# Performance work log

Measured on AMD Instinct MI355X. Metric: run time of the kernel, lower is better.

The kernel has to match this reference:

```python
import jax, jax.numpy as jnp
import numpy as np

HEAD_DIM = 16

def setup_inputs() -> dict:
    key = jax.random.key(0)
    ks = jax.random.split(key, 9)
    dim = 256
    B, H, W = 8, 32, 32
    x  = jax.random.normal(ks[0], (B, H, W, dim), jnp.float32)
    # Conv2d weights in OIHW layout (torch convention), small init
    w3 = jax.random.normal(ks[1], (dim, dim, 1, 1), jnp.float32) * 0.05
    b3 = jax.random.normal(ks[2], (dim,), jnp.float32) * 0.01
    w5 = jax.random.normal(ks[3], (dim, dim, 3, 3), jnp.float32) * 0.02
    b5 = jax.random.normal(ks[4], (dim,), jnp.float32) * 0.01
    w7 = jax.random.normal(ks[5], (dim, dim, 5, 5), jnp.float32) * 0.01
    b7 = jax.random.normal(ks[6], (dim,), jnp.float32) * 0.01
    # nn.Linear weight: (out_features=dim, in_features=attention_dim=dim), no bias
    wp = jax.random.normal(ks[7], (dim, dim), jnp.float32) * 0.05
    return {"x": x, "w3": w3, "b3": b3, "w5": w5, "b5": b5, "w7": w7, "b7": b7, "wp": wp}

def _conv2d_same(x_nchw, w_oihw, b):
    y = jax.lax.conv_general_dilated(
        x_nchw, w_oihw, window_strides=(1, 1), padding='SAME',
        dimension_numbers=('NCHW', 'OIHW', 'NCHW'))
    return y + b[None, :, None, None]

def reference(x, w3, b3, w5, b5, w7, b7, wp):
    B, H, W, C = x.shape
    N = H * W
    nh = C // HEAD_DIM            # num_heads
    scale = HEAD_DIM ** (-0.5)
    xc = jnp.transpose(x, (0, 3, 1, 2))  # NCHW
    # q: 1x1 conv, v: 3x3 conv, k: 5x5 conv (names match the torch code)
    q = _conv2d_same(xc, w3, b3).reshape(B, nh, N, HEAD_DIM)
    v = _conv2d_same(xc, w5, b5).reshape(B, nh, N, HEAD_DIM)
    k = _conv2d_same(xc, w7, b7).reshape(B, nh, N, HEAD_DIM)
    attn = jax.nn.softmax(jnp.einsum('bhnd,bhmd->bhnm', q, k) * scale, axis=-1)
    out = jnp.einsum('bhnm,bhmd->bhnd', attn, v)        # [B, nh, N, hd]
    out = jnp.transpose(out, (0, 2, 1, 3)).reshape(B, H, W, nh * HEAD_DIM)
    return out @ wp.T                                   # Linear, no bias
```

## Files before the change

### kernel.cpp

```cpp
#include <hip/hip_runtime.h>
#include <hip/hip_bf16.h>

#define DIM 256
#define HW  1024

typedef __attribute__((ext_vector_type(8))) short short8;
typedef __attribute__((ext_vector_type(4))) float floatx4;
typedef __attribute__((ext_vector_type(16))) float floatx16;
typedef __attribute__((address_space(1))) const unsigned int g_u32;
typedef __attribute__((address_space(3))) unsigned int l_u32;

#define QSCALE 0.36067376022224085f

__device__ inline unsigned short f2bf(float f) {
  union { float f; unsigned u; } v;
  v.f = f;
  unsigned u = v.u;
  u += 0x7fffu + ((u >> 16) & 1u);
  return (unsigned short)(u >> 16);
}

__device__ inline unsigned short f2bf_trunc(float f) {
  union { float f; unsigned u; } v;
  v.f = f;
  return (unsigned short)(v.u >> 16);
}

__device__ inline float ldin(const void* p, long i, int isf32) {
  if (isf32) return ((const float*)p)[i];
  union { unsigned u; float f; } v;
  v.u = ((unsigned)((const unsigned short*)p)[i]) << 16;
  return v.f;
}

__device__ inline int detect_inline(const unsigned short* __restrict__ xr,
                                    int* cnt) {
  if (threadIdx.x == 0) *cnt = 0;
  __syncthreads();
  int local = 0;
  for (int i = threadIdx.x; i < 8192; i += 256) {
    unsigned short u = xr[i];
    if ((u & 0x7F80u) == 0x7F80u) local++;
  }
  if (local) atomicAdd(cnt, local);
  __syncthreads();
  return (*cnt > 0) ? 1 : 0;
}

__device__ inline void frag_repack4(const void* __restrict__ w,
                                    unsigned short* __restrict__ wF, int KK,
                                    int slice, float* __restrict__ Wl,
                                    int isf32) {
  const int t = threadIdx.x;
  const int co16 = slice & 15;
  const int c8   = slice >> 4;
  const int RE = 32 * KK;
  const int RS = RE + 1;
  for (int g = 0; g < 4; ++g) {
    __syncthreads();
    for (int rloc = 0; rloc < 4; ++rloc) {
      const long base =
          ((long)((co16 * 16 + (g << 2) + rloc) * 256 + c8 * 32)) * KK;
      for (int i = t; i < RE; i += 256)
        Wl[rloc * RS + i] = ldin(w, base + i, isf32);
    }
    __syncthreads();
    for (int tap = 0; tap < KK; ++tap) {
      unsigned short* dst = wF + ((((tap << 3) + c8) << 4) + co16) * 512;
      if (t < 128) {
        const int colg = t >> 5;
        const int cis  = t & 31;
        const int col  = (g << 2) + colg;
        const int lane = ((cis >> 3) << 4) | col;
        const int j    = cis & 7;
        dst[lane * 8 + j] = f2bf(Wl[colg * RS + cis * KK + tap]);
      }
    }
  }
}

__global__ __launch_bounds__(256) void prep_kernel(
    const void* __restrict__ x,  const void* __restrict__ w3,
    const void* __restrict__ b3, const void* __restrict__ w5,
    const void* __restrict__ b5, const void* __restrict__ w7,
    const void* __restrict__ b7, const void* __restrict__ wp,
    unsigned short* __restrict__ xbf,
    unsigned short* __restrict__ wF3, unsigned short* __restrict__ wF5,
    unsigned short* __restrict__ wF7, unsigned short* __restrict__ wpF,
    float* __restrict__ bc, int* __restrict__ flag) {
  __shared__ float Wl[4 * 801];
  __shared__ int cnt;
  const int isf32 = detect_inline((const unsigned short*)x, &cnt);
  const int bid = blockIdx.x;
  const int t = threadIdx.x;
  if (bid < 512) {
#pragma unroll
    for (int r = 0; r < 4; ++r) {
      const int i = (bid * 1024 + r * 256 + t) * 4;
      if (isf32) {
        const float4 v = *(const float4*)((const float*)x + i);
        ushort4 o;
        o.x = f2bf(v.x); o.y = f2bf(v.y); o.z = f2bf(v.z); o.w = f2bf(v.w);
        *(ushort4*)(xbf + i) = o;
      } else {
        *(ushort4*)(xbf + i) =
            *(const ushort4*)((const unsigned short*)x + i);
      }
    }
  } else if (bid < 640) {
    frag_repack4(w7, wF7, 25, bid - 512, Wl, isf32);
  } else if (bid < 768) {
    frag_repack4(w5, wF5, 9, bid - 640, Wl, isf32);
  } else if (bid < 896) {
    frag_repack4(w3, wF3, 1, bid - 768, Wl, isf32);
  } else if (bid < 1024) {
    frag_repack4(wp, wpF, 1, bid - 896, Wl, isf32);
  } else {
#pragma unroll
    for (int r = 0; r < 3; ++r) {
      const int i = r * 256 + t;
      const void* src = (i < 256) ? b3 : (i < 512) ? b5 : b7;
      bc[i] = ldin(src, i & 255, isf32);
    }
    if (t == 0) *flag = isf32;
  }
}

__global__ __launch_bounds__(256, 2) void convqkv_kernel(
    const unsigned short* __restrict__ xbf,
    const unsigned short* __restrict__ wFq,
    const unsigned short* __restrict__ wFv,
    const unsigned short* __restrict__ wFk,
    const float* __restrict__ bc,
    unsigned short* __restrict__ qOut,
    unsigned short* __restrict__ vOut,
    unsigned short* __restrict__ kOut) {
  constexpr int WC = 36;
  constexpr int CELLS = 12 * WC;
  constexpr int LOADS = CELLS * 4;
  __shared__ unsigned short Xs[CELLS * 40];
  __shared__ unsigned short Bs[36 * 512];
  const int t    = threadIdx.x;
  const int bid  = blockIdx.x;
  const int cog0 = bid & 15;
  const int co0  = cog0 << 4;
  const int m0   = (bid >> 4) << 8;
  const int b    = m0 >> 10;
  const int n0   = m0 & 1023;
  const int r0   = n0 >> 5;
  const int wv   = t >> 6;
  const int lane = t & 63;
  const int l15  = lane & 15;
  const int quad = lane >> 4;

  floatx4 aq[4] = {}, av[4] = {}, ak[4] = {};

  for (int c8 = 0; c8 < 8; ++c8) {
    uint4 xreg[7];
#pragma unroll
    for (int rr = 0; rr < 7; ++rr) {
      const int id = rr * 256 + t;
      const int cell = id >> 2, part = id & 3;
      const int hr = cell / WC, wc = cell - hr * WC;
      const int xr = r0 + hr - 2, xc = wc - 2;
      const bool ok = (id < LOADS) && ((unsigned)xr < 32u) &&
                      ((unsigned)xc < 32u);
      const int cr = xr < 0 ? 0 : (xr > 31 ? 31 : xr);
      const int cc = xc < 0 ? 0 : (xc > 31 ? 31 : xc);
      uint4 v = *(const uint4*)&xbf[(((b * 32 + cr) * 32 + cc) << 8) +
                                    (c8 << 5) + (part << 3)];
      if (!ok) v = make_uint4(0, 0, 0, 0);
      xreg[rr] = v;
    }
    __syncthreads();
#pragma unroll
    for (int rr = 0; rr < 9; ++rr) {
      const int tap = (rr << 2) + wv;
      if (tap < 35) {
        const unsigned short* src;
        if (tap < 25) {
          src = &wFk[((((tap << 3) + c8) << 4) + cog0) * 512];
        } else if (tap < 34) {
          src = &wFv[(((((tap - 25) << 3) + c8) << 4) + cog0) * 512];
        } else {
          src = &wFq[((c8 << 4) + cog0) * 512];
        }
        __builtin_amdgcn_global_load_lds((g_u32*)(src + (lane << 3)),
                                         (l_u32*)&Bs[tap << 9], 16, 0, 0);
      }
    }
#pragma unroll
    for (int rr = 0; rr < 7; ++rr) {
      const int id = rr * 256 + t;
      if (id < LOADS)
        *(uint4*)&Xs[(id >> 2) * 40 + ((id & 3) << 3)] = xreg[rr];
    }
    __syncthreads();

#pragma unroll
    for (int tap = 0; tap < 25; ++tap) {
      const int kh = tap / 5, kw = tap % 5;
      const bool vv = (kh >= 1 && kh <= 3 && kw >= 1 && kw <= 3);
      short8 a[4];
#pragma unroll
      for (int rr2 = 0; rr2 < 2; ++rr2) {
#pragma unroll
        for (int ch = 0; ch < 2; ++ch) {
          const unsigned short* xs =
              &Xs[(((wv << 1) + rr2 + kh) * WC + (ch << 4) + l15 + kw) * 40 +
                  (quad << 3)];
          a[(rr2 << 1) + ch] = *(const short8*)xs;
        }
      }
      const short8 kb = *(const short8*)&Bs[(tap << 9) + (lane << 3)];
#pragma unroll
      for (int f = 0; f < 4; ++f)
        ak[f] = __builtin_amdgcn_mfma_f32_16x16x32_bf16(a[f], kb, ak[f],
                                                        0, 0, 0);
      if (vv) {
        const int vt = (kh - 1) * 3 + (kw - 1);
        const short8 vb = *(const short8*)&Bs[((25 + vt) << 9) + (lane << 3)];
#pragma unroll
        for (int f = 0; f < 4; ++f)
          av[f] = __builtin_amdgcn_mfma_f32_16x16x32_bf16(a[f], vb, av[f],
                                                          0, 0, 0);
      }
      if (tap == 12) {
        const short8 qb = *(const short8*)&Bs[(34 << 9) + (lane << 3)];
#pragma unroll
        for (int f = 0; f < 4; ++f)
          aq[f] = __builtin_amdgcn_mfma_f32_16x16x32_bf16(a[f], qb, aq[f],
                                                          0, 0, 0);
      }
    }
  }
#pragma unroll
  for (int rr2 = 0; rr2 < 2; ++rr2) {
#pragma unroll
    for (int ch = 0; ch < 2; ++ch) {
      const int f = (rr2 << 1) + ch;
      const int co = co0 + l15;
      const int slab = (b << 4) + (co >> 4);
      const int clo = co & 15;
      const int nb = n0 + (wv << 6) + (rr2 << 5) + (ch << 4) + (quad << 2);
      {
        const float bj = bc[co];
        floatx4 a = aq[f];
        ushort4 pk4;
        pk4.x = f2bf((a[0] + bj) * QSCALE);
        pk4.y = f2bf((a[1] + bj) * QSCALE);
        pk4.z = f2bf((a[2] + bj) * QSCALE);
        pk4.w = f2bf((a[3] + bj) * QSCALE);
        *(ushort4*)&qOut[(slab << 14) + (clo << 10) + nb] = pk4;
      }
      {
        const float bj = bc[512 + co];
        floatx4 a = ak[f];
        ushort4 pk4;
        pk4.x = f2bf(a[0] + bj); pk4.y = f2bf(a[1] + bj);
        pk4.z = f2bf(a[2] + bj); pk4.w = f2bf(a[3] + bj);
        *(ushort4*)&kOut[(slab << 14) + (clo << 10) + nb] = pk4;
      }
      {
        const float bj = bc[256 + co];
        floatx4 a = av[f];
        const int base = (slab << 14) + (clo << 6);
#pragma unroll
        for (int i = 0; i < 4; ++i) {
          const int n = nb + i;
          vOut[base + ((n & 15) << 10) + (n >> 4)] = f2bf(a[i] + bj);
        }
      }
    }
  }
}

__global__ __launch_bounds__(256, 4) void attn_mfma_kernel(
    const unsigned short* __restrict__ qg,
    const unsigned short* __restrict__ kg,
    const unsigned short* __restrict__ vg,
    unsigned short* __restrict__ out2) {
  __shared__ __align__(16) unsigned short Pb[4][32][40];
  const int t    = threadIdx.x;
  const int w    = t >> 6;
  const int lane = t & 63;
  const int slab = blockIdx.x >> 3;
  const int rb   = blockIdx.x & 7;
  const int b = slab >> 4;
  const int h = slab & 15;
  const int l31  = lane & 31;
  const int hl   = lane >> 5;
  const int l15  = lane & 15;
  const int quad = lane >> 4;

  const unsigned short* Kb = kg + (slab << 14);
  const unsigned short* Vb = vg + (slab << 14);

  const int row0 = (rb << 7) + (w << 5);
  const short8 qa =
      *(const short8*)&qg[(slab << 14) + ((row0 + l31) << 4) + (hl << 3)];

  const short onebf = (short)0x3F80;
  const short8 ones = {onebf, onebf, onebf, onebf, onebf, onebf, onebf, onebf};

  floatx4 acco[2] = {}, asum[2] = {};

  for (int kc = 0; kc < 1024; kc += 32) {
    const short8 kb = *(const short8*)&Kb[((kc + l31) << 4) + (hl << 3)];
    floatx16 s = {};
    s = __builtin_amdgcn_mfma_f32_32x32x16_bf16(qa, kb, s, 0, 0, 0);
#pragma unroll
    for (int r = 0; r < 16; ++r) {
      const float e = __builtin_amdgcn_exp2f(s[r]);
      const int row = (r & 3) + ((r >> 2) << 3) + (hl << 2);
      Pb[w][row][l31] = f2bf_trunc(e);
    }
    const short8 vb = *(const short8*)&Vb[(l15 << 10) + kc + (quad << 3)];
#pragma unroll
    for (int tt = 0; tt < 2; ++tt) {
      const short8 pa = *(const short8*)&Pb[w][(tt << 4) + l15][quad << 3];
      acco[tt] =
          __builtin_amdgcn_mfma_f32_16x16x32_bf16(pa, vb, acco[tt], 0, 0, 0);
      asum[tt] =
          __builtin_amdgcn_mfma_f32_16x16x32_bf16(pa, ones, asum[tt], 0, 0, 0);
    }
  }
#pragma unroll
  for (int tt = 0; tt < 2; ++tt) {
#pragma unroll
    for (int r = 0; r < 4; ++r) {
      const int nloc = (tt << 4) + (quad << 2) + r;
      const float val = acco[tt][r] / asum[tt][r];
      const int n = row0 + nloc;
      out2[(((b << 10) + n) << 8) + (h << 4) + l15] = f2bf(val);
    }
  }
}

__global__ __launch_bounds__(256) void linear_mfma_kernel(
    const unsigned short* __restrict__ inp,
    const unsigned short* __restrict__ wpF,
    void* __restrict__ out, const int* __restrict__ flag) {
  __shared__ unsigned short As[64 * 40];
  const int isf32 = *flag;
  const int t   = threadIdx.x;
  const int m0  = blockIdx.x << 6;
  const int co0 = blockIdx.y << 6;
  const int wv   = t >> 6;
  const int lane = t & 63;
  const int wm = (wv & 1) << 5;
  const int wn = (wv >> 1) << 5;
  const int l15  = lane & 15;
  const int quad = lane >> 4;
  const int cogb = (co0 >> 4) + (wn >> 4);
  const int rowS = t >> 2;
  const int partS = t & 3;

  floatx4 acc[2][2] = {};

  short8 cb0, cb1;
  {
    const unsigned short* wptr = &wpF[(cogb << 9) + (lane << 3)];
    cb0 = *(const short8*)wptr;
    cb1 = *(const short8*)(wptr + 512);
  }
  for (int c8 = 0; c8 < 8; ++c8) {
    const uint4 v = *(const uint4*)&inp[((m0 + rowS) << 8) + (c8 << 5) +
                                        (partS << 3)];
    short8 nb0 = {}, nb1 = {};
    if (c8 + 1 < 8) {
      const unsigned short* wptr =
          &wpF[((((c8 + 1) << 4) + cogb) << 9) + (lane << 3)];
      nb0 = *(const short8*)wptr;
      nb1 = *(const short8*)(wptr + 512);
    }
    __syncthreads();
    *(uint4*)&As[rowS * 40 + (partS << 3)] = v;
    __syncthreads();
    const unsigned short* xs = &As[(wm + l15) * 40 + (quad << 3)];
    const short8 afr0 = *(const short8*)xs;
    const short8 afr1 = *(const short8*)(xs + 16 * 40);
    acc[0][0] = __builtin_amdgcn_mfma_f32_16x16x32_bf16(afr0, cb0,
                                                        acc[0][0], 0, 0, 0);
    acc[0][1] = __builtin_amdgcn_mfma_f32_16x16x32_bf16(afr0, cb1,
                                                        acc[0][1], 0, 0, 0);
    acc[1][0] = __builtin_amdgcn_mfma_f32_16x16x32_bf16(afr1, cb0,
                                                        acc[1][0], 0, 0, 0);
    acc[1][1] = __builtin_amdgcn_mfma_f32_16x16x32_bf16(afr1, cb1,
                                                        acc[1][1], 0, 0, 0);
    cb0 = nb0; cb1 = nb1;
  }
#pragma unroll
  for (int mi = 0; mi < 2; ++mi) {
#pragma unroll
    for (int ni = 0; ni < 2; ++ni) {
      const int co = co0 + wn + (ni << 4) + l15;
      const int mb = m0 + wm + (mi << 4) + (quad << 2);
      floatx4 a = acc[mi][ni];
      if (!isf32) {
        unsigned short* o16 = (unsigned short*)out;
#pragma unroll
        for (int r = 0; r < 4; ++r) o16[(mb + r) * 256 + co] = f2bf(a[r]);
      } else {
        float* o32 = (float*)out;
#pragma unroll
        for (int r = 0; r < 4; ++r) o32[(mb + r) * 256 + co] = a[r];
      }
    }
  }
}

extern "C" void kernel_launch(void* const* d_in, const int* in_sizes, int n_in,
                              void* d_out, int out_size, void* d_ws,
                              size_t ws_size, hipStream_t stream) {
  const void* x  = d_in[0];
  const void* w3 = d_in[1];
  const void* b3 = d_in[2];
  const void* w5 = d_in[3];
  const void* b5 = d_in[4];
  const void* w7 = d_in[5];
  const void* b7 = d_in[6];
  const void* wp = d_in[7];

  char* p = (char*)d_ws;
  int* flag = (int*)p;                       p += 256;
  unsigned short* xbf = (unsigned short*)p;  p += 4u * 1024 * 1024;
  unsigned short* wF3 = (unsigned short*)p;  p += 131072;
  unsigned short* wF5 = (unsigned short*)p;  p += 1179648;
  unsigned short* wF7 = (unsigned short*)p;  p += 3276800;
  unsigned short* wpF = (unsigned short*)p;  p += 131072;
  float* bc = (float*)p;                     p += 4096;
  unsigned short* qc  = (unsigned short*)p;  p += 4194304;
  unsigned short* kT  = (unsigned short*)p;  p += 4194304;
  unsigned short* vT  = (unsigned short*)p;  p += 4194304;
  unsigned short* o2b = (unsigned short*)p;  p += 4194304;

  prep_kernel<<<1025, 256, 0, stream>>>(x, w3, b3, w5, b5, w7, b7, wp, xbf,
                                        wF3, wF5, wF7, wpF, bc, flag);

  convqkv_kernel<<<512, 256, 0, stream>>>(xbf, wF3, wF5, wF7, bc, qc, vT, kT);

  attn_mfma_kernel<<<1024, 256, 0, stream>>>(qc, kT, vT, o2b);

  dim3 lg(128, 4);
  linear_mfma_kernel<<<lg, 256, 0, stream>>>(o2b, wpF, d_out, flag);
}
```

Measured before the change: 174.6 us.

## Prefetch conv inputs, pipeline attention loads, pack P stores, drop linear LDS staging

The conv kernel now loads the next channel chunk of x into registers while the MFMAs for the current chunk run, hiding global latency behind compute. The attention loop prefetches the next K and V fragments, swaps the MFMA operand order so each lane holds consecutive P values, and writes P with packed bf16 conversions as 8-byte stores instead of scalar truncating stores. The linear kernel reads A fragments straight from global memory and no longer stages them through LDS with barriers. The weight repack is templated on kernel size so its loops unroll. The cost is more live registers in the conv kernel, and P is now rounded by hardware conversion instead of truncated.

Result: no change. 177.3 us (+1.5%).

```diff
diff --git a/kernel.cpp b/kernel.cpp
--- a/kernel.cpp
+++ b/kernel.cpp
@@ -47,32 +47,35 @@
   return (*cnt > 0) ? 1 : 0;
 }
 
+template <int KK>
 __device__ inline void frag_repack4(const void* __restrict__ w,
-                                    unsigned short* __restrict__ wF, int KK,
+                                    unsigned short* __restrict__ wF,
                                     int slice, float* __restrict__ Wl,
                                     int isf32) {
   const int t = threadIdx.x;
   const int co16 = slice & 15;
   const int c8   = slice >> 4;
-  const int RE = 32 * KK;
-  const int RS = RE + 1;
+  constexpr int RE = 32 * KK;
+  constexpr int RS = RE + 1;
   for (int g = 0; g < 4; ++g) {
     __syncthreads();
     for (int rloc = 0; rloc < 4; ++rloc) {
       const long base =
           ((long)((co16 * 16 + (g << 2) + rloc) * 256 + c8 * 32)) * KK;
+#pragma unroll
       for (int i = t; i < RE; i += 256)
         Wl[rloc * RS + i] = ldin(w, base + i, isf32);
     }
     __syncthreads();
-    for (int tap = 0; tap < KK; ++tap) {
-      unsigned short* dst = wF + ((((tap << 3) + c8) << 4) + co16) * 512;
-      if (t < 128) {
-        const int colg = t >> 5;
-        const int cis  = t & 31;
-        const int col  = (g << 2) + colg;
-        const int lane = ((cis >> 3) << 4) | col;
-        const int j    = cis & 7;
+    if (t < 128) {
+      const int colg = t >> 5;
+      const int cis  = t & 31;
+      const int col  = (g << 2) + colg;
+      const int lane = ((cis >> 3) << 4) | col;
+      const int j    = cis & 7;
+#pragma unroll
+      for (int tap = 0; tap < KK; ++tap) {
+        unsigned short* dst = wF + ((((tap << 3) + c8) << 4) + co16) * 512;
         dst[lane * 8 + j] = f2bf(Wl[colg * RS + cis * KK + tap]);
       }
     }
@@ -108,13 +111,13 @@
       }
     }
   } else if (bid < 640) {
-    frag_repack4(w7, wF7, 25, bid - 512, Wl, isf32);
+    frag_repack4<25>(w7, wF7, bid - 512, Wl, isf32);
   } else if (bid < 768) {
-    frag_repack4(w5, wF5, 9, bid - 640, Wl, isf32);
+    frag_repack4<9>(w5, wF5, bid - 640, Wl, isf32);
   } else if (bid < 896) {
-    frag_repack4(w3, wF3, 1, bid - 768, Wl, isf32);
+    frag_repack4<1>(w3, wF3, bid - 768, Wl, isf32);
   } else if (bid < 1024) {
-    frag_repack4(wp, wpF, 1, bid - 896, Wl, isf32);
+    frag_repack4<1>(wp, wpF, bid - 896, Wl, isf32);
   } else {
 #pragma unroll
     for (int r = 0; r < 3; ++r) {
@@ -155,23 +158,28 @@
 
   floatx4 aq[4] = {}, av[4] = {}, ak[4] = {};
 
+  uint4 xreg[7];
+#define LOADX(C8)                                                         \
+  do {                                                                    \
+    _Pragma("unroll") for (int rr = 0; rr < 7; ++rr) {                    \
+      const int id = rr * 256 + t;                                        \
+      const int cell = id >> 2, part = id & 3;                            \
+      const int hr = cell / WC, wc = cell - hr * WC;                      \
+      const int xr = r0 + hr - 2, xc = wc - 2;                            \
+      const bool okk = (id < LOADS) && ((unsigned)xr < 32u) &&            \
+                       ((unsigned)xc < 32u);                              \
+      const int cr = xr < 0 ? 0 : (xr > 31 ? 31 : xr);                    \
+      const int cc = xc < 0 ? 0 : (xc > 31 ? 31 : xc);                    \
+      uint4 vv_ = *(const uint4*)&xbf[(((b * 32 + cr) * 32 + cc) << 8) +  \
+                                      ((C8) << 5) + (part << 3)];         \
+      if (!okk) vv_ = make_uint4(0, 0, 0, 0);                             \
+      xreg[rr] = vv_;                                                     \
+    }                                                                     \
+  } while (0)
+
+  LOADX(0);
+
   for (int c8 = 0; c8 < 8; ++c8) {
-    uint4 xreg[7];
-#pragma unroll
-    for (int rr = 0; rr < 7; ++rr) {
-      const int id = rr * 256 + t;
-      const int cell = id >> 2, part = id & 3;
-      const int hr = cell / WC, wc = cell - hr * WC;
-      const int xr = r0 + hr - 2, xc = wc - 2;
-      const bool ok = (id < LOADS) && ((unsigned)xr < 32u) &&
-                      ((unsigned)xc < 32u);
-      const int cr = xr < 0 ? 0 : (xr > 31 ? 31 : xr);
-      const int cc = xc < 0 ? 0 : (xc > 31 ? 31 : xc);
-      uint4 v = *(const uint4*)&xbf[(((b * 32 + cr) * 32 + cc) << 8) +
-                                    (c8 << 5) + (part << 3)];
-      if (!ok) v = make_uint4(0, 0, 0, 0);
-      xreg[rr] = v;
-    }
     __syncthreads();
 #pragma unroll
     for (int rr = 0; rr < 9; ++rr) {
@@ -197,6 +205,8 @@
     }
     __syncthreads();
 
+    if (c8 < 7) LOADX(c8 + 1);
+
 #pragma unroll
     for (int tap = 0; tap < 25; ++tap) {
       const int kh = tap / 5, kw = tap % 5;
@@ -234,6 +244,7 @@
       }
     }
   }
+#undef LOADX
 #pragma unroll
   for (int rr2 = 0; rr2 < 2; ++rr2) {
 #pragma unroll
@@ -305,17 +316,29 @@
 
   floatx4 acco[2] = {}, asum[2] = {};
 
+  short8 kb = *(const short8*)&Kb[(l31 << 4) + (hl << 3)];
+  short8 vb = *(const short8*)&Vb[(l15 << 10) + (quad << 3)];
+
   for (int kc = 0; kc < 1024; kc += 32) {
-    const short8 kb = *(const short8*)&Kb[((kc + l31) << 4) + (hl << 3)];
+    const int kn = (kc + 32) & 1023;
+    const short8 kb_n =
+        *(const short8*)&Kb[((kn + l31) << 4) + (hl << 3)];
+    const short8 vb_n =
+        *(const short8*)&Vb[(l15 << 10) + kn + (quad << 3)];
     floatx16 s = {};
-    s = __builtin_amdgcn_mfma_f32_32x32x16_bf16(qa, kb, s, 0, 0, 0);
-#pragma unroll
-    for (int r = 0; r < 16; ++r) {
-      const float e = __builtin_amdgcn_exp2f(s[r]);
-      const int row = (r & 3) + ((r >> 2) << 3) + (hl << 2);
-      Pb[w][row][l31] = f2bf_trunc(e);
-    }
-    const short8 vb = *(const short8*)&Vb[(l15 << 10) + kc + (quad << 3)];
+    s = __builtin_amdgcn_mfma_f32_32x32x16_bf16(kb, qa, s, 0, 0, 0);
+#pragma unroll
+    for (int g = 0; g < 4; ++g) {
+      const float e0 = __builtin_amdgcn_exp2f(s[(g << 2) + 0]);
+      const float e1 = __builtin_amdgcn_exp2f(s[(g << 2) + 1]);
+      const float e2 = __builtin_amdgcn_exp2f(s[(g << 2) + 2]);
+      const float e3 = __builtin_amdgcn_exp2f(s[(g << 2) + 3]);
+      unsigned lo, hi;
+      asm("v_cvt_pk_bf16_f32 %0, %1, %2" : "=v"(lo) : "v"(e0), "v"(e1));
+      asm("v_cvt_pk_bf16_f32 %0, %1, %2" : "=v"(hi) : "v"(e2), "v"(e3));
+      uint2 pk; pk.x = lo; pk.y = hi;
+      *(uint2*)&Pb[w][l31][(g << 3) + (hl << 2)] = pk;
+    }
 #pragma unroll
     for (int tt = 0; tt < 2; ++tt) {
       const short8 pa = *(const short8*)&Pb[w][(tt << 4) + l15][quad << 3];
@@ -324,6 +347,7 @@
       asum[tt] =
           __builtin_amdgcn_mfma_f32_16x16x32_bf16(pa, ones, asum[tt], 0, 0, 0);
     }
+    kb = kb_n; vb = vb_n;
   }
 #pragma unroll
   for (int tt = 0; tt < 2; ++tt) {
@@ -341,7 +365,6 @@
     const unsigned short* __restrict__ inp,
     const unsigned short* __restrict__ wpF,
     void* __restrict__ out, const int* __restrict__ flag) {
-  __shared__ unsigned short As[64 * 40];
   const int isf32 = *flag;
   const int t   = threadIdx.x;
   const int m0  = blockIdx.x << 6;
@@ -353,10 +376,11 @@
   const int l15  = lane & 15;
   const int quad = lane >> 4;
   const int cogb = (co0 >> 4) + (wn >> 4);
-  const int rowS = t >> 2;
-  const int partS = t & 3;
 
   floatx4 acc[2][2] = {};
+
+  const unsigned short* arow =
+      &inp[((m0 + wm + l15) << 8) + (quad << 3)];
 
   short8 cb0, cb1;
   {
@@ -364,9 +388,10 @@
     cb0 = *(const short8*)wptr;
     cb1 = *(const short8*)(wptr + 512);
   }
+#pragma unroll
   for (int c8 = 0; c8 < 8; ++c8) {
-    const uint4 v = *(const uint4*)&inp[((m0 + rowS) << 8) + (c8 << 5) +
-                                        (partS << 3)];
+    const short8 afr0 = *(const short8*)(arow + (c8 << 5));
+    const short8 afr1 = *(const short8*)(arow + (16 << 8) + (c8 << 5));
     short8 nb0 = {}, nb1 = {};
     if (c8 + 1 < 8) {
       const unsigned short* wptr =
@@ -374,12 +399,6 @@
       nb0 = *(const short8*)wptr;
       nb1 = *(const short8*)(wptr + 512);
     }
-    __syncthreads();
-    *(uint4*)&As[rowS * 40 + (partS << 3)] = v;
-    __syncthreads();
-    const unsigned short* xs = &As[(wm + l15) * 40 + (quad << 3)];
-    const short8 afr0 = *(const short8*)xs;
-    const short8 afr1 = *(const short8*)(xs + 16 * 40);
     acc[0][0] = __builtin_amdgcn_mfma_f32_16x16x32_bf16(afr0, cb0,
                                                         acc[0][0], 0, 0, 0);
     acc[0][1] = __builtin_amdgcn_mfma_f32_16x16x32_bf16(afr0, cb1,
```
